# Performance work log

Measured on AMD Instinct MI355X. Metric: run time of the kernel, lower is better.

The kernel has to match this reference:

```python
import jax, jax.numpy as jnp
import numpy as np

NUM_PRIMITIVES = 1024
DIM = 1024
TAU = 0.5  # temperature used by LivingCodebook.discretize default


def setup_inputs() -> dict:
    key = jax.random.key(0)
    k1, k2 = jax.random.split(key)
    logits = jax.random.normal(k1, (8, 4096, NUM_PRIMITIVES), dtype=jnp.float32)
    # learned codebook (nn.Parameter torch.randn(K, D) * 0.02)
    primitives = jax.random.normal(k2, (NUM_PRIMITIVES, DIM), dtype=jnp.float32) * 0.02
    return {"logits": logits, "primitives": primitives}


def _gumbel_softmax_hard(logits, key, tau):
    # F.gumbel_softmax(logits, tau, hard=True): straight-through one-hot
    g = jax.random.gumbel(key, logits.shape, dtype=logits.dtype)
    y_soft = jax.nn.softmax((logits + g) / tau, axis=-1)  # [b,s,k]
    idx = jnp.argmax(y_soft, axis=-1)                     # [b,s]
    y_hard = jax.nn.one_hot(idx, logits.shape[-1], dtype=logits.dtype)
    # hard forward value, soft gradient
    y = y_hard + y_soft - jax.lax.stop_gradient(y_soft)
    return y, idx


def reference(logits, primitives):
    """LivingCodebook.discretize: hard gumbel-softmax selection + codebook gather
    (expressed as one-hot GEMM for straight-through grads), plus the
    activation_count update vectorized as a scatter-add."""
    noise_key = jax.random.key(42)
    weights, indices = _gumbel_softmax_hard(logits, noise_key, TAU)
    # embeddings = weights @ primitives : [b,s,k] x [k,d] -> [b,s,d]
    embeddings = jnp.einsum("bsk,kd->bsd", weights, primitives)
    # activation_count[idx] += 1 for every selected index (vectorized)
    counts = jnp.zeros((primitives.shape[0],), dtype=jnp.int32).at[indices.reshape(-1)].add(1)
    return embeddings, indices, counts
```

## Files before the change

kernel.cpp:

```cpp
#include <hip/hip_runtime.h>
#include <stdint.h>

#define NROWS   32768
#define KDIM    1024
#define EMB_OFF 33554432
#define IDX_OFF 33554432
#define CNT_OFF 33587200

__device__ __forceinline__ uint32_t rotl32(uint32_t x, int r) {
    return (x << r) | (x >> (32 - r));
}

__device__ __forceinline__ uint32_t threefry_bits(uint32_t ctr) {
    const uint32_t ks0 = 0u;
    const uint32_t ks1 = 42u;
    const uint32_t ks2 = 0x1BD11BDAu ^ 0u ^ 42u;

    uint32_t x0 = 0u + ks0;
    uint32_t x1 = ctr + ks1;

    x0 += x1; x1 = rotl32(x1, 13); x1 ^= x0;
    x0 += x1; x1 = rotl32(x1, 15); x1 ^= x0;
    x0 += x1; x1 = rotl32(x1, 26); x1 ^= x0;
    x0 += x1; x1 = rotl32(x1,  6); x1 ^= x0;
    x0 += ks1; x1 += ks2 + 1u;
    x0 += x1; x1 = rotl32(x1, 17); x1 ^= x0;
    x0 += x1; x1 = rotl32(x1, 29); x1 ^= x0;
    x0 += x1; x1 = rotl32(x1, 16); x1 ^= x0;
    x0 += x1; x1 = rotl32(x1, 24); x1 ^= x0;
    x0 += ks2; x1 += ks0 + 2u;
    x0 += x1; x1 = rotl32(x1, 13); x1 ^= x0;
    x0 += x1; x1 = rotl32(x1, 15); x1 ^= x0;
    x0 += x1; x1 = rotl32(x1, 26); x1 ^= x0;
    x0 += x1; x1 = rotl32(x1,  6); x1 ^= x0;
    x0 += ks0; x1 += ks1 + 3u;
    x0 += x1; x1 = rotl32(x1, 17); x1 ^= x0;
    x0 += x1; x1 = rotl32(x1, 29); x1 ^= x0;
    x0 += x1; x1 = rotl32(x1, 16); x1 ^= x0;
    x0 += x1; x1 = rotl32(x1, 24); x1 ^= x0;
    x0 += ks1; x1 += ks2 + 4u;
    x0 += x1; x1 = rotl32(x1, 13); x1 ^= x0;
    x0 += x1; x1 = rotl32(x1, 15); x1 ^= x0;
    x0 += x1; x1 = rotl32(x1, 26); x1 ^= x0;
    x0 += x1; x1 = rotl32(x1,  6); x1 ^= x0;
    x0 += ks2; x1 += ks0 + 5u;

    return x0 ^ x1;
}

__device__ __forceinline__ float gumbel_from_bits(uint32_t bits) {
    float f = __uint_as_float((bits >> 9) | 0x3f800000u) - 1.0f;
    float u = fmaxf(f, 1.17549435e-38f);
    return -logf(-logf(u));
}

__global__ __launch_bounds__(256) void gumbel_argmax_gather(
    const float* __restrict__ logits,
    const float* __restrict__ prim,
    float* __restrict__ out,
    int* __restrict__ counts)
{
    const int row = blockIdx.x;
    const int tid = threadIdx.x;
    const uint32_t base = (uint32_t)row * (uint32_t)KDIM;

    float bv = -INFINITY;
    int   bk = 0;
    #pragma unroll
    for (int m = 0; m < 4; ++m) {
        const int k = tid + m * 256;
        const uint32_t ctr = base + (uint32_t)k;
        const float g = gumbel_from_bits(threefry_bits(ctr));
        const float z = logits[base + (uint32_t)k] + g;
        if (z > bv) { bv = z; bk = k; }
    }

    #pragma unroll
    for (int off = 32; off > 0; off >>= 1) {
        const float ov = __shfl_down(bv, off);
        const int   ok = __shfl_down(bk, off);
        if (ov > bv || (ov == bv && ok < bk)) { bv = ov; bk = ok; }
    }

    __shared__ float s_v[4];
    __shared__ int   s_k[4];
    __shared__ int   s_idx;
    const int wave = tid >> 6;
    if ((tid & 63) == 0) { s_v[wave] = bv; s_k[wave] = bk; }
    __syncthreads();

    if (tid == 0) {
        float v = s_v[0]; int kk = s_k[0];
        #pragma unroll
        for (int w = 1; w < 4; ++w) {
            if (s_v[w] > v || (s_v[w] == v && s_k[w] < kk)) { v = s_v[w]; kk = s_k[w]; }
        }
        s_idx = kk;
        out[IDX_OFF + row] = (float)kk;
        atomicAdd(&counts[kk], 1);
    }
    __syncthreads();

    const int idx = s_idx;
    const float4* __restrict__ src = (const float4*)(prim + (size_t)idx * KDIM);
    float4* __restrict__ dst = (float4*)(out + (size_t)row * KDIM);
    dst[tid] = src[tid];
}

__global__ void counts_to_float(const int* __restrict__ counts, float* __restrict__ out) {
    const int t = blockIdx.x * blockDim.x + threadIdx.x;
    if (t < KDIM) out[t] = (float)counts[t];
}

extern "C" void kernel_launch(void* const* d_in, const int* in_sizes, int n_in,
                              void* d_out, int out_size, void* d_ws, size_t ws_size,
                              hipStream_t stream) {
    const float* logits = (const float*)d_in[0];
    const float* prim   = (const float*)d_in[1];
    float* out = (float*)d_out;
    int*   cnt = (int*)d_ws;

    hipMemsetAsync(d_ws, 0, KDIM * sizeof(int), stream);

    gumbel_argmax_gather<<<NROWS, 256, 0, stream>>>(logits, prim, out, cnt);
    counts_to_float<<<4, 256, 0, stream>>>(cnt, out + CNT_OFF);
}
```

Measured before the change: 250.9 us.

## Use log2-domain Gumbel scoring, vectorized logit loads, and direct float count atomics

Replaces the two accurate logf calls with hardware log2 intrinsics, plus a polynomial for log(u) when u is near 1, and compares scores scaled by 1/ln2, which leaves the argmax unchanged. Each thread now loads four contiguous logits as one float4 instead of four strided scalars. Counts are accumulated as float atomics directly into the output, which removes the int workspace and the conversion kernel launch. The approximate log may flip argmax ties in rare near-equal cases.

After: 242.6 us. -3.3%, faster.

```diff
diff --git a/kernel.cpp b/kernel.cpp
--- a/kernel.cpp
+++ b/kernel.cpp
@@ -3,7 +3,6 @@
 
 #define NROWS   32768
 #define KDIM    1024
-#define EMB_OFF 33554432
 #define IDX_OFF 33554432
 #define CNT_OFF 33587200
 
@@ -48,31 +47,44 @@
     return x0 ^ x1;
 }
 
-__device__ __forceinline__ float gumbel_from_bits(uint32_t bits) {
-    float f = __uint_as_float((bits >> 9) | 0x3f800000u) - 1.0f;
-    float u = fmaxf(f, 1.17549435e-38f);
-    return -logf(-logf(u));
+__device__ __forceinline__ float score_from_bits(uint32_t bits, float logit) {
+    float v1 = __uint_as_float((bits >> 9) | 0x3f800000u);
+    float f  = v1 - 1.0f;
+    float u  = fmaxf(f, 1.17549435e-38f);
+    float w  = u - 1.0f;
+    float q;
+    q = fmaf(w, -0.20609929f,  0.24044917f);
+    q = fmaf(w, q, -0.28853901f);
+    q = fmaf(w, q,  0.36067376f);
+    q = fmaf(w, q, -0.48089835f);
+    q = fmaf(w, q,  0.72134752f);
+    q = fmaf(w, q, -1.44269504f);
+    float tp = w * q;
+    float th = -__builtin_amdgcn_logf(u);
+    float t  = (u >= 0.875f) ? tp : th;
+    float lg = __builtin_amdgcn_logf(t);
+    return fmaf(logit, 1.44269504f, -lg);
 }
 
 __global__ __launch_bounds__(256) void gumbel_argmax_gather(
     const float* __restrict__ logits,
     const float* __restrict__ prim,
-    float* __restrict__ out,
-    int* __restrict__ counts)
+    float* __restrict__ out)
 {
     const int row = blockIdx.x;
     const int tid = threadIdx.x;
     const uint32_t base = (uint32_t)row * (uint32_t)KDIM;
+    const uint32_t k0   = 4u * (uint32_t)tid;
+
+    const float4 l4 = *reinterpret_cast<const float4*>(logits + base + k0);
+    const float lv[4] = {l4.x, l4.y, l4.z, l4.w};
 
     float bv = -INFINITY;
     int   bk = 0;
     #pragma unroll
     for (int m = 0; m < 4; ++m) {
-        const int k = tid + m * 256;
-        const uint32_t ctr = base + (uint32_t)k;
-        const float g = gumbel_from_bits(threefry_bits(ctr));
-        const float z = logits[base + (uint32_t)k] + g;
-        if (z > bv) { bv = z; bk = k; }
+        const float z = score_from_bits(threefry_bits(base + k0 + (uint32_t)m), lv[m]);
+        if (z > bv) { bv = z; bk = (int)k0 + m; }
     }
 
     #pragma unroll
@@ -97,7 +109,7 @@
         }
         s_idx = kk;
         out[IDX_OFF + row] = (float)kk;
-        atomicAdd(&counts[kk], 1);
+        atomicAdd(out + CNT_OFF + kk, 1.0f);
     }
     __syncthreads();
 
@@ -107,21 +119,14 @@
     dst[tid] = src[tid];
 }
 
-__global__ void counts_to_float(const int* __restrict__ counts, float* __restrict__ out) {
-    const int t = blockIdx.x * blockDim.x + threadIdx.x;
-    if (t < KDIM) out[t] = (float)counts[t];
-}
-
 extern "C" void kernel_launch(void* const* d_in, const int* in_sizes, int n_in,
                               void* d_out, int out_size, void* d_ws, size_t ws_size,
                               hipStream_t stream) {
     const float* logits = (const float*)d_in[0];
     const float* prim   = (const float*)d_in[1];
     float* out = (float*)d_out;
-    int*   cnt = (int*)d_ws;
+    (void)d_ws; (void)ws_size; (void)in_sizes; (void)n_in; (void)out_size;
 
-    hipMemsetAsync(d_ws, 0, KDIM * sizeof(int), stream);
-
-    gumbel_argmax_gather<<<NROWS, 256, 0, stream>>>(logits, prim, out, cnt);
-    counts_to_float<<<4, 256, 0, stream>>>(cnt, out + CNT_OFF);
+    hipMemsetAsync(out + CNT_OFF, 0, KDIM * sizeof(float), stream);
+    gumbel_argmax_gather<<<NROWS, 256, 0, stream>>>(logits, prim, out);
 }
```
